# Optimization experiments

Hardware: AMD Instinct MI355X
Metric: run time of the kernel (lower is better)

## Reference

```python
import jax, jax.numpy as jnp
import numpy as np


def setup_inputs() -> dict:
    key = jax.random.key(0)
    k1, k2 = jax.random.split(key)
    pred = jax.random.normal(k1, (4, 8192, 3), dtype=jnp.float32)
    target = jax.random.normal(k2, (4, 8192, 3), dtype=jnp.float32)
    return {"pred": pred, "target": target}


def reference(pred, target):
    # Pairwise squared distances via the expansion ||p-q||^2 = ||p||^2 + ||q||^2 - 2 p.q
    # Avoids materializing the O(B*M*N*3) diff tensor of the naive broadcast.
    p_sq = jnp.sum(pred * pred, axis=-1)          # [B, M]
    q_sq = jnp.sum(target * target, axis=-1)      # [B, N]
    cross = jnp.einsum("bmd,bnd->bmn", pred, target)  # [B, M, N]
    dist_sq = p_sq[:, :, None] + q_sq[:, None, :] - 2.0 * cross  # [B, M, N]
    min_dist_pred = jnp.min(dist_sq, axis=2).mean(axis=1)    # [B] min over target per pred point
    min_dist_target = jnp.min(dist_sq, axis=1).mean(axis=1)  # [B] min over pred per target point
    return jnp.mean(min_dist_pred + min_dist_target)
```

## Files before the change

### kernel.cpp

```cpp
#include <hip/hip_runtime.h>


#define THREADS 512
#define P 8
#define S 32
#define G 128
#define TILE 64
#define LSTRIDE (TILE + 1)

typedef float float2_t __attribute__((ext_vector_type(2)));
typedef float float4_t __attribute__((ext_vector_type(4)));

static __device__ __forceinline__ float2_t pk_fma_bl_bh(float2_t a, float2_t b) {
  float2_t d;
  asm("v_pk_fma_f32 %0, %1, %2, %2 op_sel:[0,0,1] op_sel_hi:[1,0,1]"
      : "=v"(d) : "v"(a), "v"(b));
  return d;
}
static __device__ __forceinline__ float2_t pk_fma_bh(float2_t a, float2_t b, float2_t c) {
  float2_t d;
  asm("v_pk_fma_f32 %0, %1, %2, %3 op_sel:[0,1,0] op_sel_hi:[1,1,1]"
      : "=v"(d) : "v"(a), "v"(b), "v"(c));
  return d;
}
static __device__ __forceinline__ float2_t pk_fma_bl(float2_t a, float2_t b, float2_t c) {
  float2_t d;
  asm("v_pk_fma_f32 %0, %1, %2, %3 op_sel:[0,0,0] op_sel_hi:[1,0,1]"
      : "=v"(d) : "v"(a), "v"(b), "v"(c));
  return d;
}

__global__ __launch_bounds__(THREADS, 4) void chamfer_min_kernel(
    const float* __restrict__ pred, const float* __restrict__ target,
    float* __restrict__ out, int M, float scale) {
  const int blocksPerDir = M / G;
  int pblk = blockIdx.x % blocksPerDir;
  int bd = blockIdx.x / blocksPerDir;
  int dir = bd & 1;
  int b = bd >> 1;
  const float* src = (dir ? target : pred) + (size_t)b * M * 3;
  const float* ref = (dir ? pred : target) + (size_t)b * M * 3;

  __shared__ float4_t lds[S * LSTRIDE];

  int t = threadIdx.x;
  int g = t >> 4;
  int l = t & 15;

  float cm[P];
  float2_t a2x[P / 2], a2y[P / 2], a2z[P / 2];
  int pbase = pblk * G;
#pragma unroll
  for (int i = 0; i < P / 2; ++i) {
    int p0 = pbase + l + 16 * (2 * i);
    int p1 = pbase + l + 16 * (2 * i + 1);
    float x0 = src[p0 * 3 + 0], y0 = src[p0 * 3 + 1], z0 = src[p0 * 3 + 2];
    float x1 = src[p1 * 3 + 0], y1 = src[p1 * 3 + 1], z1 = src[p1 * 3 + 2];
    cm[2 * i] = x0 * x0 + y0 * y0 + z0 * z0;
    cm[2 * i + 1] = x1 * x1 + y1 * y1 + z1 * z1;
    a2x[i] = (float2_t){-2.f * x0, -2.f * x1};
    a2y[i] = (float2_t){-2.f * y0, -2.f * y1};
    a2z[i] = (float2_t){-2.f * z0, -2.f * z1};
  }
  float mlo[P / 2], mhi[P / 2];
#pragma unroll
  for (int i = 0; i < P / 2; ++i) { mlo[i] = 3.0e38f; mhi[i] = 3.0e38f; }

  const int sliceLen = M / S;
  const int ntiles = sliceLen / TILE;
  for (int k = 0; k < ntiles; ++k) {
    __syncthreads();
#pragma unroll
    for (int i = 0; i < (S * TILE) / THREADS; ++i) {
      int idx = t + THREADS * i;
      int s = idx >> 6;
      int jj = idx & (TILE - 1);
      int n = s * sliceLen + k * TILE + jj;
      float qx = ref[n * 3 + 0], qy = ref[n * 3 + 1], qz = ref[n * 3 + 2];
      lds[s * LSTRIDE + jj] =
          (float4_t){qx, qy, qz, qx * qx + qy * qy + qz * qz};
    }
    __syncthreads();
    const float4_t* tp = lds + g * LSTRIDE;
#pragma unroll 2
    for (int j = 0; j < TILE; j += 4) {
      float4_t q0 = tp[j + 0];
      float4_t q1 = tp[j + 1];
      float4_t q2 = tp[j + 2];
      float4_t q3 = tp[j + 3];
      float2_t q0xy = __builtin_shufflevector(q0, q0, 0, 1);
      float2_t q0zw = __builtin_shufflevector(q0, q0, 2, 3);
      float2_t q1xy = __builtin_shufflevector(q1, q1, 0, 1);
      float2_t q1zw = __builtin_shufflevector(q1, q1, 2, 3);
      float2_t q2xy = __builtin_shufflevector(q2, q2, 0, 1);
      float2_t q2zw = __builtin_shufflevector(q2, q2, 2, 3);
      float2_t q3xy = __builtin_shufflevector(q3, q3, 0, 1);
      float2_t q3zw = __builtin_shufflevector(q3, q3, 2, 3);
#pragma unroll
      for (int i = 0; i < P / 2; ++i) {
        float2_t d0 = pk_fma_bl(a2x[i], q0xy,
                        pk_fma_bh(a2y[i], q0xy, pk_fma_bl_bh(a2z[i], q0zw)));
        float2_t d1 = pk_fma_bl(a2x[i], q1xy,
                        pk_fma_bh(a2y[i], q1xy, pk_fma_bl_bh(a2z[i], q1zw)));
        float2_t d2 = pk_fma_bl(a2x[i], q2xy,
                        pk_fma_bh(a2y[i], q2xy, pk_fma_bl_bh(a2z[i], q2zw)));
        float2_t d3 = pk_fma_bl(a2x[i], q3xy,
                        pk_fma_bh(a2y[i], q3xy, pk_fma_bl_bh(a2z[i], q3zw)));
        mlo[i] = fminf(fminf(mlo[i], d0.x), d1.x);
        mlo[i] = fminf(fminf(mlo[i], d2.x), d3.x);
        mhi[i] = fminf(fminf(mhi[i], d0.y), d1.y);
        mhi[i] = fminf(fminf(mhi[i], d2.y), d3.y);
      }
    }
  }

  __syncthreads();
  float* lmin = (float*)lds;
  float* lcm = (float*)lds + S * G;
#pragma unroll
  for (int i = 0; i < P / 2; ++i) {
    lmin[g * G + (l + 16 * (2 * i))] = mlo[i];
    lmin[g * G + (l + 16 * (2 * i + 1))] = mhi[i];
    if (g == 0) {
      lcm[l + 16 * (2 * i)] = cm[2 * i];
      lcm[l + 16 * (2 * i + 1)] = cm[2 * i + 1];
    }
  }
  __syncthreads();
  float v = 0.f;
  if (t < G) {
    float mn = 3.0e38f;
#pragma unroll
    for (int s = 0; s < S; ++s) mn = fminf(mn, lmin[s * G + t]);
    v = lcm[t] + mn;
  }
  for (int off = 32; off > 0; off >>= 1) v += __shfl_down(v, off, 64);
  __shared__ float ws[THREADS / 64];
  if ((t & 63) == 0) ws[t >> 6] = v;
  __syncthreads();
  if (t == 0) {
    float bsum = 0.f;
#pragma unroll
    for (int w = 0; w < THREADS / 64; ++w) bsum += ws[w];
    atomicAdd(out, bsum * scale);
  }
}

extern "C" void kernel_launch(void* const* d_in, const int* in_sizes, int n_in,
                              void* d_out, int out_size, void* d_ws,
                              size_t ws_size, hipStream_t stream) {
  const float* pred = (const float*)d_in[0];
  const float* target = (const float*)d_in[1];
  float* out = (float*)d_out;
  const int B = 4;
  const int M = in_sizes[0] / (B * 3);

  float scale = 1.0f / (float)(B * M);

  hipMemsetAsync(out, 0, sizeof(float), stream);
  int blocks = B * 2 * (M / G);
  chamfer_min_kernel<<<blocks, THREADS, 0, stream>>>(pred, target, out, M,
                                                     scale);
}
```

Before: 96.88 us.

## Bucket-sort points by x and prune Chamfer search to a bounded x-window

Adds a pre-pass that bucket-sorts each point cloud by x into 1024 buckets, storing float4 points with their squared norm plus per-bucket offsets in the workspace. Each min block then scans only reference points whose x lies near its own x-range. From that partial scan it takes the largest current min distance as a radius W, and scans the extra points within W in x. This removes most of the all-pairs distance work while staying exact. The cost is an extra single-block-per-cloud sort kernel with shared-memory atomics, plus more barriers and a two-phase scan.

```diff
diff --git a/kernel.cpp b/kernel.cpp
--- a/kernel.cpp
+++ b/kernel.cpp
@@ -1,147 +1,235 @@
 #include <hip/hip_runtime.h>
 
+
+typedef float float2_t __attribute__((ext_vector_type(2)));
+typedef float float4_t __attribute__((ext_vector_type(4)));
+
+#define NB 1024
+#define XLO_BND -4.5f
+#define XSCALE (NB / 9.0f)
+
+static __device__ __forceinline__ int bucket_of(float x) {
+  float f = (x - XLO_BND) * XSCALE;
+  f = fminf(fmaxf(f, 0.f), (float)(NB - 1));
+  return (int)f;
+}
+
+static __device__ __forceinline__ float2_t pk_fma_bl_bh(float2_t a, float2_t b) {
+  float2_t d;
+  asm("v_pk_fma_f32 %0, %1, %2, %2 op_sel:[0,0,1] op_sel_hi:[1,0,1]"
+      : "=v"(d) : "v"(a), "v"(b));
+  return d;
+}
+static __device__ __forceinline__ float2_t pk_fma_bh(float2_t a, float2_t b, float2_t c) {
+  float2_t d;
+  asm("v_pk_fma_f32 %0, %1, %2, %3 op_sel:[0,1,0] op_sel_hi:[1,1,1]"
+      : "=v"(d) : "v"(a), "v"(b), "v"(c));
+  return d;
+}
+static __device__ __forceinline__ float2_t pk_fma_bl(float2_t a, float2_t b, float2_t c) {
+  float2_t d;
+  asm("v_pk_fma_f32 %0, %1, %2, %3 op_sel:[0,0,0] op_sel_hi:[1,0,1]"
+      : "=v"(d) : "v"(a), "v"(b), "v"(c));
+  return d;
+}
+
+__global__ __launch_bounds__(1024) void bucket_sort_kernel(
+    const float* __restrict__ pred, const float* __restrict__ target,
+    float4_t* __restrict__ sorted, int* __restrict__ bstart, int M) {
+  int c = blockIdx.x;
+  int b = c >> 1;
+  const float* src = ((c & 1) ? target : pred) + (size_t)b * M * 3;
+  __shared__ int hist[NB], sc[NB], cur[NB];
+  int t = threadIdx.x;
+  hist[t] = 0;
+  __syncthreads();
+  for (int i = t; i < M; i += 1024)
+    atomicAdd(&hist[bucket_of(src[3 * i])], 1);
+  __syncthreads();
+  sc[t] = hist[t];
+  __syncthreads();
+  for (int off = 1; off < NB; off <<= 1) {
+    int v = sc[t];
+    if (t >= off) v += sc[t - off];
+    __syncthreads();
+    sc[t] = v;
+    __syncthreads();
+  }
+  int excl = sc[t] - hist[t];
+  bstart[c * (NB + 1) + t] = excl;
+  if (t == 0) bstart[c * (NB + 1) + NB] = M;
+  cur[t] = excl;
+  __syncthreads();
+  for (int i = t; i < M; i += 1024) {
+    float x = src[3 * i], y = src[3 * i + 1], z = src[3 * i + 2];
+    int slot = atomicAdd(&cur[bucket_of(x)], 1);
+    sorted[(size_t)c * M + slot] = (float4_t){x, y, z, x * x + y * y + z * z};
+  }
+}
 
 #define THREADS 512
 #define P 8
 #define S 32
 #define G 128
 #define TILE 64
+#define CHUNK (S * TILE)
 #define LSTRIDE (TILE + 1)
 
-typedef float float2_t __attribute__((ext_vector_type(2)));
-typedef float float4_t __attribute__((ext_vector_type(4)));
-
-static __device__ __forceinline__ float2_t pk_fma_bl_bh(float2_t a, float2_t b) {
-  float2_t d;
-  asm("v_pk_fma_f32 %0, %1, %2, %2 op_sel:[0,0,1] op_sel_hi:[1,0,1]"
-      : "=v"(d) : "v"(a), "v"(b));
-  return d;
-}
-static __device__ __forceinline__ float2_t pk_fma_bh(float2_t a, float2_t b, float2_t c) {
-  float2_t d;
-  asm("v_pk_fma_f32 %0, %1, %2, %3 op_sel:[0,1,0] op_sel_hi:[1,1,1]"
-      : "=v"(d) : "v"(a), "v"(b), "v"(c));
-  return d;
-}
-static __device__ __forceinline__ float2_t pk_fma_bl(float2_t a, float2_t b, float2_t c) {
-  float2_t d;
-  asm("v_pk_fma_f32 %0, %1, %2, %3 op_sel:[0,0,0] op_sel_hi:[1,0,1]"
-      : "=v"(d) : "v"(a), "v"(b), "v"(c));
-  return d;
-}
-
-__global__ __launch_bounds__(THREADS, 4) void chamfer_min_kernel(
-    const float* __restrict__ pred, const float* __restrict__ target,
+__global__ __launch_bounds__(THREADS) void chamfer_min_kernel(
+    const float4_t* __restrict__ sorted, const int* __restrict__ bstart,
     float* __restrict__ out, int M, float scale) {
-  const int blocksPerDir = M / G;
+  int blocksPerDir = M / G;
   int pblk = blockIdx.x % blocksPerDir;
   int bd = blockIdx.x / blocksPerDir;
   int dir = bd & 1;
   int b = bd >> 1;
-  const float* src = (dir ? target : pred) + (size_t)b * M * 3;
-  const float* ref = (dir ? pred : target) + (size_t)b * M * 3;
+  const float4_t* SP = sorted + (size_t)(2 * b + dir) * M;
+  const float4_t* RP = sorted + (size_t)(2 * b + (dir ^ 1)) * M;
 
   __shared__ float4_t lds[S * LSTRIDE];
+  __shared__ float pmin[S][G];
+  __shared__ int bst[NB + 1];
+  __shared__ float red[16];
+  __shared__ int wsqb;
 
   int t = threadIdx.x;
   int g = t >> 4;
   int l = t & 15;
 
+  for (int i = t; i < NB + 1; i += THREADS)
+    bst[i] = bstart[(2 * b + (dir ^ 1)) * (NB + 1) + i];
+
   float cm[P];
   float2_t a2x[P / 2], a2y[P / 2], a2z[P / 2];
+  float xmn = 3.0e38f, xmx = -3.0e38f;
   int pbase = pblk * G;
 #pragma unroll
   for (int i = 0; i < P / 2; ++i) {
-    int p0 = pbase + l + 16 * (2 * i);
-    int p1 = pbase + l + 16 * (2 * i + 1);
-    float x0 = src[p0 * 3 + 0], y0 = src[p0 * 3 + 1], z0 = src[p0 * 3 + 2];
-    float x1 = src[p1 * 3 + 0], y1 = src[p1 * 3 + 1], z1 = src[p1 * 3 + 2];
-    cm[2 * i] = x0 * x0 + y0 * y0 + z0 * z0;
-    cm[2 * i + 1] = x1 * x1 + y1 * y1 + z1 * z1;
-    a2x[i] = (float2_t){-2.f * x0, -2.f * x1};
-    a2y[i] = (float2_t){-2.f * y0, -2.f * y1};
-    a2z[i] = (float2_t){-2.f * z0, -2.f * z1};
-  }
+    float4_t v0 = SP[pbase + l + 16 * (2 * i)];
+    float4_t v1 = SP[pbase + l + 16 * (2 * i + 1)];
+    cm[2 * i] = v0.w;
+    cm[2 * i + 1] = v1.w;
+    a2x[i] = (float2_t){-2.f * v0.x, -2.f * v1.x};
+    a2y[i] = (float2_t){-2.f * v0.y, -2.f * v1.y};
+    a2z[i] = (float2_t){-2.f * v0.z, -2.f * v1.z};
+    xmn = fminf(xmn, fminf(v0.x, v1.x));
+    xmx = fmaxf(xmx, fmaxf(v0.x, v1.x));
+  }
+  for (int off = 32; off > 0; off >>= 1) {
+    xmn = fminf(xmn, __shfl_down(xmn, off, 64));
+    xmx = fmaxf(xmx, __shfl_down(xmx, off, 64));
+  }
+  if ((t & 63) == 0) { red[t >> 6] = xmn; red[8 + (t >> 6)] = xmx; }
+  if (t == 0) wsqb = 0;
+  __syncthreads();
+  xmn = red[0]; xmx = red[8];
+#pragma unroll
+  for (int w = 1; w < THREADS / 64; ++w) {
+    xmn = fminf(xmn, red[w]);
+    xmx = fmaxf(xmx, red[8 + w]);
+  }
+
   float mlo[P / 2], mhi[P / 2];
 #pragma unroll
   for (int i = 0; i < P / 2; ++i) { mlo[i] = 3.0e38f; mhi[i] = 3.0e38f; }
 
-  const int sliceLen = M / S;
-  const int ntiles = sliceLen / TILE;
-  for (int k = 0; k < ntiles; ++k) {
-    __syncthreads();
-#pragma unroll
-    for (int i = 0; i < (S * TILE) / THREADS; ++i) {
-      int idx = t + THREADS * i;
-      int s = idx >> 6;
-      int jj = idx & (TILE - 1);
-      int n = s * sliceLen + k * TILE + jj;
-      float qx = ref[n * 3 + 0], qy = ref[n * 3 + 1], qz = ref[n * 3 + 2];
-      lds[s * LSTRIDE + jj] =
-          (float4_t){qx, qy, qz, qx * qx + qy * qy + qz * qz};
-    }
-    __syncthreads();
-    const float4_t* tp = lds + g * LSTRIDE;
+  auto scan_range = [&](int lo, int hi) {
+    for (int t0 = lo; t0 < hi; t0 += CHUNK) {
+      __syncthreads();
+#pragma unroll
+      for (int r = 0; r < CHUNK / THREADS; ++r) {
+        int e = t + THREADS * r;
+        int gi = t0 + e;
+        float4_t v = (gi < hi) ? RP[gi] : (float4_t){0.f, 0.f, 0.f, 3.0e38f};
+        lds[(e >> 6) * LSTRIDE + (e & 63)] = v;
+      }
+      __syncthreads();
+      if (t0 + TILE * g < hi) {
+        const float4_t* tp = lds + g * LSTRIDE;
 #pragma unroll 2
-    for (int j = 0; j < TILE; j += 4) {
-      float4_t q0 = tp[j + 0];
-      float4_t q1 = tp[j + 1];
-      float4_t q2 = tp[j + 2];
-      float4_t q3 = tp[j + 3];
-      float2_t q0xy = __builtin_shufflevector(q0, q0, 0, 1);
-      float2_t q0zw = __builtin_shufflevector(q0, q0, 2, 3);
-      float2_t q1xy = __builtin_shufflevector(q1, q1, 0, 1);
-      float2_t q1zw = __builtin_shufflevector(q1, q1, 2, 3);
-      float2_t q2xy = __builtin_shufflevector(q2, q2, 0, 1);
-      float2_t q2zw = __builtin_shufflevector(q2, q2, 2, 3);
-      float2_t q3xy = __builtin_shufflevector(q3, q3, 0, 1);
-      float2_t q3zw = __builtin_shufflevector(q3, q3, 2, 3);
-#pragma unroll
-      for (int i = 0; i < P / 2; ++i) {
-        float2_t d0 = pk_fma_bl(a2x[i], q0xy,
-                        pk_fma_bh(a2y[i], q0xy, pk_fma_bl_bh(a2z[i], q0zw)));
-        float2_t d1 = pk_fma_bl(a2x[i], q1xy,
-                        pk_fma_bh(a2y[i], q1xy, pk_fma_bl_bh(a2z[i], q1zw)));
-        float2_t d2 = pk_fma_bl(a2x[i], q2xy,
-                        pk_fma_bh(a2y[i], q2xy, pk_fma_bl_bh(a2z[i], q2zw)));
-        float2_t d3 = pk_fma_bl(a2x[i], q3xy,
-                        pk_fma_bh(a2y[i], q3xy, pk_fma_bl_bh(a2z[i], q3zw)));
-        mlo[i] = fminf(fminf(mlo[i], d0.x), d1.x);
-        mlo[i] = fminf(fminf(mlo[i], d2.x), d3.x);
-        mhi[i] = fminf(fminf(mhi[i], d0.y), d1.y);
-        mhi[i] = fminf(fminf(mhi[i], d2.y), d3.y);
+        for (int j = 0; j < TILE; j += 4) {
+          float4_t q0 = tp[j + 0];
+          float4_t q1 = tp[j + 1];
+          float4_t q2 = tp[j + 2];
+          float4_t q3 = tp[j + 3];
+          float2_t q0xy = __builtin_shufflevector(q0, q0, 0, 1);
+          float2_t q0zw = __builtin_shufflevector(q0, q0, 2, 3);
+          float2_t q1xy = __builtin_shufflevector(q1, q1, 0, 1);
+          float2_t q1zw = __builtin_shufflevector(q1, q1, 2, 3);
+          float2_t q2xy = __builtin_shufflevector(q2, q2, 0, 1);
+          float2_t q2zw = __builtin_shufflevector(q2, q2, 2, 3);
+          float2_t q3xy = __builtin_shufflevector(q3, q3, 0, 1);
+          float2_t q3zw = __builtin_shufflevector(q3, q3, 2, 3);
+#pragma unroll
+          for (int i = 0; i < P / 2; ++i) {
+            float2_t d0 = pk_fma_bl(a2x[i], q0xy,
+                            pk_fma_bh(a2y[i], q0xy, pk_fma_bl_bh(a2z[i], q0zw)));
+            float2_t d1 = pk_fma_bl(a2x[i], q1xy,
+                            pk_fma_bh(a2y[i], q1xy, pk_fma_bl_bh(a2z[i], q1zw)));
+            float2_t d2 = pk_fma_bl(a2x[i], q2xy,
+                            pk_fma_bh(a2y[i], q2xy, pk_fma_bl_bh(a2z[i], q2zw)));
+            float2_t d3 = pk_fma_bl(a2x[i], q3xy,
+                            pk_fma_bh(a2y[i], q3xy, pk_fma_bl_bh(a2z[i], q3zw)));
+            mlo[i] = fminf(fminf(mlo[i], d0.x), d1.x);
+            mlo[i] = fminf(fminf(mlo[i], d2.x), d3.x);
+            mhi[i] = fminf(fminf(mhi[i], d0.y), d1.y);
+            mhi[i] = fminf(fminf(mhi[i], d2.y), d3.y);
+          }
+        }
       }
     }
-  }
-
-  __syncthreads();
-  float* lmin = (float*)lds;
-  float* lcm = (float*)lds + S * G;
+  };
+
+  int kb0 = bucket_of(xmn) - 4; if (kb0 < 0) kb0 = 0;
+  int kb1 = bucket_of(xmx) + 4; if (kb1 > NB - 1) kb1 = NB - 1;
+  int ilo = bst[kb0], ihi = bst[kb1 + 1];
+  scan_range(ilo, ihi);
+
+  __syncthreads();
 #pragma unroll
   for (int i = 0; i < P / 2; ++i) {
-    lmin[g * G + (l + 16 * (2 * i))] = mlo[i];
-    lmin[g * G + (l + 16 * (2 * i + 1))] = mhi[i];
-    if (g == 0) {
-      lcm[l + 16 * (2 * i)] = cm[2 * i];
-      lcm[l + 16 * (2 * i + 1)] = cm[2 * i + 1];
-    }
+    pmin[g][l + 16 * (2 * i)] = mlo[i];
+    pmin[g][l + 16 * (2 * i + 1)] = mhi[i];
+  }
+  __syncthreads();
+  if (t < G) {
+    float mn = 3.0e38f;
+#pragma unroll
+    for (int s = 0; s < S; ++s) mn = fminf(mn, pmin[s][t]);
+    float dd = fmaxf(cm[t >> 4] + mn, 0.f);
+    atomicMax(&wsqb, __float_as_int(dd));
+  }
+  __syncthreads();
+  float W = sqrtf(__int_as_float(wsqb));
+
+  int jlo = bst[bucket_of(xmn - W)];
+  int jhi = bst[bucket_of(xmx + W) + 1];
+  if (jlo > ilo) jlo = ilo;
+  if (jhi < ihi) jhi = ihi;
+  scan_range(jlo, ilo);
+  scan_range(ihi, jhi);
+
+  __syncthreads();
+#pragma unroll
+  for (int i = 0; i < P / 2; ++i) {
+    pmin[g][l + 16 * (2 * i)] = mlo[i];
+    pmin[g][l + 16 * (2 * i + 1)] = mhi[i];
   }
   __syncthreads();
   float v = 0.f;
   if (t < G) {
     float mn = 3.0e38f;
 #pragma unroll
-    for (int s = 0; s < S; ++s) mn = fminf(mn, lmin[s * G + t]);
-    v = lcm[t] + mn;
+    for (int s = 0; s < S; ++s) mn = fminf(mn, pmin[s][t]);
+    v = cm[t >> 4] + mn;
   }
   for (int off = 32; off > 0; off >>= 1) v += __shfl_down(v, off, 64);
-  __shared__ float ws[THREADS / 64];
-  if ((t & 63) == 0) ws[t >> 6] = v;
+  if ((t & 63) == 0) red[t >> 6] = v;
   __syncthreads();
   if (t == 0) {
     float bsum = 0.f;
 #pragma unroll
-    for (int w = 0; w < THREADS / 64; ++w) bsum += ws[w];
+    for (int w = 0; w < THREADS / 64; ++w) bsum += red[w];
     atomicAdd(out, bsum * scale);
   }
 }
@@ -155,10 +243,13 @@
   const int B = 4;
   const int M = in_sizes[0] / (B * 3);
 
+  float4_t* sorted = (float4_t*)d_ws;
+  int* bstart = (int*)((char*)d_ws + (size_t)2 * B * M * 16);
+
   float scale = 1.0f / (float)(B * M);
-
   hipMemsetAsync(out, 0, sizeof(float), stream);
-  int blocks = B * 2 * (M / G);
-  chamfer_min_kernel<<<blocks, THREADS, 0, stream>>>(pred, target, out, M,
-                                                     scale);
-}
+
+  bucket_sort_kernel<<<2 * B, 1024, 0, stream>>>(pred, target, sorted, bstart, M);
+  chamfer_min_kernel<<<B * 2 * (M / G), THREADS, 0, stream>>>(sorted, bstart,
+                                                              out, M, scale);
+}
```

New measurement: 112.9 us. 16.6% more time.
